# Optimization experiments

Measured on AMD Instinct MI355X. Metric: run time of the kernel, lower is better.

Reference implementation:

```python
import jax, jax.numpy as jnp
import numpy as np

H = 16      # num_attention_heads
D = 128     # head_size
ROT = 32    # rotary_ndims
WIN = 256   # attention_window[layer_id]
G = 64      # max_global_tokens
BASE = 10000.0


def _rotate_half(x):
    x1, x2 = jnp.split(x, 2, axis=-1)
    return jnp.concatenate([-x2, x1], axis=-1)


def setup_inputs() -> dict:
    key = jax.random.key(0)
    ks = jax.random.split(key, 6)
    B, S, HD = 2, 2048, H * D
    hidden_states = jax.random.normal(ks[0], (B, S, HD), jnp.float32)
    attention_mask = jnp.zeros((B, 1, 1, S), jnp.float32)
    glob_idx = jnp.sort(jax.random.randint(ks[1], (B, G), 0, S), axis=-1)
    W_qkv = jax.random.normal(ks[2], (HD, 3 * HD), jnp.float32) * 0.02
    b_qkv = jnp.zeros((3 * HD,), jnp.float32)
    W_o = jax.random.normal(ks[3], (HD, HD), jnp.float32) * 0.02
    b_o = jnp.zeros((HD,), jnp.float32)
    return {"hidden_states": hidden_states, "attention_mask": attention_mask,
            "glob_idx": glob_idx, "W_qkv": W_qkv, "b_qkv": b_qkv,
            "W_o": W_o, "b_o": b_o}


def reference(hidden_states, attention_mask, glob_idx, W_qkv, b_qkv, W_o, b_o):
    B, S, HD = hidden_states.shape
    qkv = (hidden_states @ W_qkv + b_qkv).reshape(B, S, H, 3 * D)
    q = qkv[..., :D].transpose(0, 2, 1, 3)        # [B,H,S,D]
    k = qkv[..., D:2 * D].transpose(0, 2, 1, 3)
    v = qkv[..., 2 * D:].transpose(0, 2, 1, 3)

    # GPT-NeoX rotary on first ROT dims
    inv_freq = 1.0 / (BASE ** (jnp.arange(0, ROT, 2, dtype=jnp.float32) / ROT))
    freqs = jnp.einsum('s,f->sf', jnp.arange(S, dtype=jnp.float32), inv_freq)
    emb = jnp.concatenate([freqs, freqs], axis=-1)           # [S,ROT]
    cos = jnp.cos(emb)[None, None]
    sin = jnp.sin(emb)[None, None]
    q = jnp.concatenate([q[..., :ROT] * cos + _rotate_half(q[..., :ROT]) * sin,
                         q[..., ROT:]], axis=-1)
    k = jnp.concatenate([k[..., :ROT] * cos + _rotate_half(k[..., :ROT]) * sin,
                         k[..., ROT:]], axis=-1)

    # step_attn path: keys/values are head-averaged before attention (key.mean(1))
    k_mean = k.mean(axis=1)   # [B,S,D]
    v_mean = v.mean(axis=1)
    scale = 1.0 / jnp.sqrt(jnp.float32(D))
    minv = jnp.finfo(jnp.float32).min

    s0 = jnp.einsum('bhqd,bkd->bhqk', q[:, :, :WIN], k_mean[:, :WIN]) * scale
    causal = jnp.tril(jnp.ones((WIN, WIN), bool))
    s0 = jnp.where(causal[None, None], s0, minv) + attention_mask[..., :WIN]
    out0 = jnp.einsum('bhqk,bkd->bhqd', jax.nn.softmax(s0, axis=-1), v_mean[:, :WIN])

    Sq = S - WIN
    steps = jnp.arange(Sq)
    win_pos = steps[:, None] + 1 + jnp.arange(WIN)[None, :]
    k_win = k_mean[:, win_pos]
    v_win = v_mean[:, win_pos]
    mask_win = attention_mask[:, 0, 0, :][:, win_pos][:, None]
    qs = q[:, :, WIN:]                                        # [B,H,Sq,D]
    s_win = jnp.einsum('bhqd,bqwd->bhqw', qs, k_win) * scale + mask_win

    k_glob = jnp.take_along_axis(k_mean, glob_idx[..., None], axis=1)  # [B,G,D]
    v_glob = jnp.take_along_axis(v_mean, glob_idx[..., None], axis=1)
    # sorted indices: 'filter < i then truncate to G' == prefix-valid mask per slot
    valid = (glob_idx[:, None, :] < steps[None, :, None])[:, None]     # [B,1,Sq,G]
    s_glob = jnp.where(valid, jnp.einsum('bhqd,bgd->bhqg', qs, k_glob) * scale, minv)

    w = jax.nn.softmax(jnp.concatenate([s_glob, s_win], axis=-1), axis=-1)
    out_steps = (jnp.einsum('bhqg,bgd->bhqd', w[..., :G], v_glob)
                 + jnp.einsum('bhqw,bqwd->bhqd', w[..., G:], v_win))

    out = jnp.concatenate([out0, out_steps], axis=2)          # [B,H,S,D]
    out = out.transpose(0, 2, 1, 3).reshape(B, S, HD)
    return out @ W_o + b_o
```

## Files before the change

kernel.cpp:

```cpp
#include <hip/hip_runtime.h>
#include <math.h>

#define SCALE_ 0.08838834764831845f
#define MINV_  (-3.4028234663852886e38f)

typedef __bf16 bf16;
typedef bf16  bf16x4 __attribute__((ext_vector_type(4)));
typedef bf16  bf16x8 __attribute__((ext_vector_type(8)));
typedef float f32x4  __attribute__((ext_vector_type(4)));
typedef float f32x16 __attribute__((ext_vector_type(16)));
typedef float float4v __attribute__((ext_vector_type(4)));

#define LD8(p) (*(const bf16x8*)(p))

__device__ __forceinline__ f32x4 mfma16(bf16x8 a, bf16x8 b, f32x4 c) {
    return __builtin_amdgcn_mfma_f32_16x16x32_bf16(a, b, c, 0, 0, 0);
}
__device__ __forceinline__ f32x16 mfma32(bf16x8 a, bf16x8 b, f32x16 c) {
    return __builtin_amdgcn_mfma_f32_32x32x16_bf16(a, b, c, 0, 0, 0);
}

typedef const __attribute__((address_space(1))) void* gas_t;
typedef __attribute__((address_space(3))) void* sas_t;
__device__ __forceinline__ void gload_lds16(const void* g, void* l) {
    __builtin_amdgcn_global_load_lds((gas_t)g, (sas_t)l, 16, 0, 0);
}

__global__ __launch_bounds__(256) void prep_kernel(const float* __restrict__ hidden, bf16* __restrict__ A16,
                                                   const float* __restrict__ Wqkv, bf16* __restrict__ BT1,
                                                   const float* __restrict__ Wo, bf16* __restrict__ BT2,
                                                   const float* __restrict__ bqkv, float* __restrict__ bias1)
{
    int x = blockIdx.x;
    if (x < 512) {
        int k0 = x * 4;
        int j = threadIdx.x;
        float acc[4];
        #pragma unroll
        for (int k = 0; k < 4; k++) acc[k] = 0.f;
        for (int h = 0; h < 16; h++) {
            #pragma unroll
            for (int k = 0; k < 4; k++)
                acc[k] += Wqkv[(size_t)(k0 + k) * 6144 + h * 384 + 128 + j];
        }
        #pragma unroll
        for (int k = 0; k < 4; k++)
            BT1[(size_t)(2048 + j) * 2048 + k0 + k] = (bf16)(acc[k] * 0.0625f);
        return;
    }
    if (x == 512) {
        for (int c = threadIdx.x; c < 2304; c += 256) {
            if (c < 2048) bias1[c] = bqkv[(c >> 7) * 384 + (c & 127)];
            else {
                int j = c - 2048; float s = 0.f;
                for (int h = 0; h < 16; h++) s += bqkv[h * 384 + 128 + j];
                bias1[c] = s * 0.0625f;
            }
        }
        return;
    }
    if (x < 8705) {
        int i = ((x - 513) * 256 + threadIdx.x) * 4;
        float4v v = *(const float4v*)(hidden + i);
        bf16x4 o; o.x = (bf16)v.x; o.y = (bf16)v.y; o.z = (bf16)v.z; o.w = (bf16)v.w;
        *(bf16x4*)(A16 + i) = o;
        return;
    }
    __shared__ float tile[32][33];
    int t = x - 8705;
    int z = t >> 12;
    int tt = t & 4095;
    const float* W = z ? Wo : Wqkv;
    bf16* BT = z ? BT2 : BT1;
    int srcStride = z ? 2048 : 6144;
    int k0 = (tt & 63) * 32, n0 = (tt >> 6) * 32;
    int c = threadIdx.x & 31, r = threadIdx.x >> 5;
    int n = n0 + c;
    int src = z ? n : ((n >> 7) * 384 + (n & 127));
    #pragma unroll
    for (int rr = 0; rr < 32; rr += 8)
        tile[r + rr][c] = W[(size_t)(k0 + r + rr) * srcStride + src];
    __syncthreads();
    #pragma unroll
    for (int rr = 0; rr < 32; rr += 8)
        BT[(size_t)(n0 + r + rr) * 2048 + k0 + c] = (bf16)tile[c][r + rr];
}


#define GEMM64K128_PROLOGUE_AND_KLOOP                                                     \
    __shared__ __align__(16) bf16 As[128 * 128];                                          \
    __shared__ __align__(16) bf16 Bs[64 * 128];                                           \
    const int tid  = threadIdx.x;                                                         \
    const int wv   = tid >> 6, lane = tid & 63, l32 = lane & 31, half = lane >> 5;        \
    const int m0 = blockIdx.y * 128, n0 = blockIdx.x * 64;                                \
    int rowSA[8], colSA[8];                                                               \
    _Pragma("unroll")                                                                     \
    for (int j = 0; j < 8; j++) {                                                         \
        int flat = (wv * 8 + j) * 64 + lane;                                              \
        rowSA[j] = flat >> 4;                                                             \
        colSA[j] = ((flat & 15) ^ (rowSA[j] & 15)) * 8;                                   \
    }                                                                                     \
    int rowSB[4], colSB[4];                                                               \
    _Pragma("unroll")                                                                     \
    for (int j = 0; j < 4; j++) {                                                         \
        int flat = (wv * 4 + j) * 64 + lane;                                              \
        rowSB[j] = flat >> 4;                                                             \
        colSB[j] = ((flat & 15) ^ (rowSB[j] & 15)) * 8;                                   \
    }                                                                                     \
    f32x16 acc[2];                                                                        \
    _Pragma("unroll")                                                                     \
    for (int i = 0; i < 2; i++)                                                           \
        _Pragma("unroll")                                                                 \
        for (int r = 0; r < 16; r++) acc[i][r] = 0.f;                                     \
    for (int kk = 0; kk < K; kk += 128) {                                                 \
        __syncthreads();                                                                  \
        _Pragma("unroll")                                                                 \
        for (int j = 0; j < 8; j++)                                                       \
            gload_lds16(A  + (size_t)(m0 + rowSA[j]) * K + kk + colSA[j], &As[(wv * 8 + j) * 512]); \
        _Pragma("unroll")                                                                 \
        for (int j = 0; j < 4; j++)                                                       \
            gload_lds16(BT + (size_t)(n0 + rowSB[j]) * K + kk + colSB[j], &Bs[(wv * 4 + j) * 512]); \
        __syncthreads();                                                                  \
        const int rowA = wv * 32 + l32;                                                   \
        const int rowB0 = l32, rowB1 = 32 + l32;                                          \
        _Pragma("unroll")                                                                 \
        for (int k16 = 0; k16 < 8; k16++) {                                               \
            int lc = k16 * 2 + half;                                                      \
            bf16x8 af = LD8(&As[rowA * 128 + ((lc ^ (rowA & 15)) * 8)]);                  \
            bf16x8 b0 = LD8(&Bs[rowB0 * 128 + ((lc ^ (rowB0 & 15)) * 8)]);                \
            bf16x8 b1 = LD8(&Bs[rowB1 * 128 + ((lc ^ (rowB1 & 15)) * 8)]);                \
            acc[0] = mfma32(af, b0, acc[0]);                                              \
            acc[1] = mfma32(af, b1, acc[1]);                                              \
        }                                                                                 \
    }

__global__ __launch_bounds__(256) void gemm_rot_kernel(const bf16* __restrict__ A, const bf16* __restrict__ BT,
                                                       const float* __restrict__ bias, bf16* __restrict__ C,
                                                       int M, int N, int K)
{
    GEMM64K128_PROLOGUE_AND_KLOOP

    #pragma unroll
    for (int nt = 0; nt < 2; nt++) {
        int n = n0 + nt * 32 + l32;
        float bn = bias[n];
        const bool rot = ((n0 & 127) == 0) && (nt == 0) && (n0 <= 2048);
        float inv = rot ? __expf(-0.575646273248511f * (float)(l32 & 15)) : 0.f;
        #pragma unroll
        for (int r = 0; r < 16; r++) {
            int m = m0 + wv * 32 + (r & 3) + 8 * (r >> 2) + 4 * half;
            float v = acc[nt][r] + bn;
            if (rot) {
                float ang = (float)(m & 2047) * inv;
                float cs, sn;
                __sincosf(ang, &sn, &cs);
                float pv = __shfl_xor(v, 16, 64);
                v = (l32 < 16) ? (v * cs - pv * sn) : (v * cs + pv * sn);
            }
            C[(size_t)m * N + n] = (bf16)v;
        }
    }
}


__global__ __launch_bounds__(256) void gemm_out_kernel(const bf16* __restrict__ A, const bf16* __restrict__ BT,
                                                       const float* __restrict__ bias, float* __restrict__ C,
                                                       int M, int N, int K)
{
    __shared__ __align__(16) bf16 As[128 * 64];
    __shared__ __align__(16) bf16 Bs[128 * 64];
    const int tid  = threadIdx.x;
    const int wv   = tid >> 6, lane = tid & 63, l32 = lane & 31, half = lane >> 5;
    const int wrow = wv >> 1, wcol = wv & 1;
    const int m0 = blockIdx.y * 128, n0 = blockIdx.x * 128;
    int rowS[4], colS[4];
    #pragma unroll
    for (int j = 0; j < 4; j++) {
        int flat = (wv * 4 + j) * 64 + lane;
        int row = flat >> 3, cp = flat & 7;
        rowS[j] = row;
        colS[j] = (cp ^ (row & 7)) * 8;
    }
    f32x16 acc[2][2];
    #pragma unroll
    for (int i = 0; i < 2; i++)
        #pragma unroll
        for (int j = 0; j < 2; j++)
            #pragma unroll
            for (int r = 0; r < 16; r++) acc[i][j][r] = 0.f;
    for (int kk = 0; kk < K; kk += 64) {
        __syncthreads();
        #pragma unroll
        for (int j = 0; j < 4; j++) {
            gload_lds16(A  + (size_t)(m0 + rowS[j]) * K + kk + colS[j], &As[(wv * 4 + j) * 512]);
            gload_lds16(BT + (size_t)(n0 + rowS[j]) * K + kk + colS[j], &Bs[(wv * 4 + j) * 512]);
        }
        __syncthreads();
        bf16x8 af[2][4], bfr[2][4];
        #pragma unroll
        for (int mt = 0; mt < 2; mt++) {
            int row = wrow * 64 + mt * 32 + l32;
            #pragma unroll
            for (int k16 = 0; k16 < 4; k16++) {
                int lc = k16 * 2 + half;
                af[mt][k16] = LD8(&As[row * 64 + ((lc ^ (row & 7)) * 8)]);
            }
        }
        #pragma unroll
        for (int nt = 0; nt < 2; nt++) {
            int row = wcol * 64 + nt * 32 + l32;
            #pragma unroll
            for (int k16 = 0; k16 < 4; k16++) {
                int lc = k16 * 2 + half;
                bfr[nt][k16] = LD8(&Bs[row * 64 + ((lc ^ (row & 7)) * 8)]);
            }
        }
        #pragma unroll
        for (int k16 = 0; k16 < 4; k16++)
            #pragma unroll
            for (int mt = 0; mt < 2; mt++)
                #pragma unroll
                for (int nt = 0; nt < 2; nt++)
                    acc[mt][nt] = mfma32(af[mt][k16], bfr[nt][k16], acc[mt][nt]);
    }

    #pragma unroll
    for (int mt = 0; mt < 2; mt++) {
        #pragma unroll
        for (int nt = 0; nt < 2; nt++) {
            int n = n0 + wcol * 64 + nt * 32 + l32;
            float bn = bias[n];
            #pragma unroll
            for (int r = 0; r < 16; r++) {
                int m = m0 + wrow * 64 + mt * 32 + (r & 3) + 8 * (r >> 2) + 4 * half;
                C[(size_t)m * N + n] = acc[mt][nt][r] + bn;
            }
        }
    }
}

__global__ __launch_bounds__(256) void pretile_kernel(const bf16* __restrict__ C1, const int* __restrict__ gidx,
                                                      bf16* __restrict__ KF, bf16* __restrict__ VF)
{
    __shared__ bf16 Vt[64][130];
    const int c = blockIdx.x, b = blockIdx.y;
    const bool isGlob = (c == 32);
    const int tid = threadIdx.x;

    {
        int row = tid >> 2, cb = (tid & 3) * 32;
        int pos = isGlob ? gidx[b * 64 + row] : (c * 64 + row);
        const bf16* src = C1 + (size_t)(b * 2048 + pos) * 2304 + 2176 + cb;
        #pragma unroll
        for (int k = 0; k < 4; k++)
            *(bf16x8*)&Vt[row][cb + k * 8] = LD8(src + k * 8);
    }
    __syncthreads();

    #pragma unroll
    for (int i = 0; i < 4; i++) {
        int sid = tid + i * 256;
        int lane = sid & 63, fi = sid >> 6;
        int l16 = lane & 15, quad = lane >> 4;
        int t = fi >> 2, ks = fi & 3;
        int pos = isGlob ? gidx[b * 64 + t * 16 + l16] : (c * 64 + t * 16 + l16);
        const bf16* src = C1 + (size_t)(b * 2048 + pos) * 2304 + 2048 + ks * 32 + quad * 8;
        *(bf16x8*)&KF[((size_t)(b * 33 + c) * 16 + fi) * 512 + lane * 8] = LD8(src);
    }

    #pragma unroll
    for (int i = 0; i < 4; i++) {
        int sid = tid + i * 256;
        int lane = sid & 63, fi = sid >> 6;
        int l16 = lane & 15, quad = lane >> 4;
        int dt = fi >> 1, ks2 = fi & 1;
        int d = dt * 16 + l16;
        bf16x8 v;
        #pragma unroll
        for (int j = 0; j < 8; j++)
            v[j] = Vt[ks2 * 32 + quad * 8 + j][d];
        *(bf16x8*)&VF[((size_t)(b * 33 + c) * 16 + fi) * 512 + lane * 8] = v;
    }
}

#define PSTRIDE 88

__device__ __forceinline__ void attn0_body(int bx, int h, int b, bf16* Pw,
                                           const bf16* __restrict__ C1, const bf16* __restrict__ KF,
                                           const bf16* __restrict__ VF, const float* __restrict__ mask,
                                           bf16* __restrict__ attn)
{
    const int tid = threadIdx.x, wv = tid >> 6, lane = tid & 63, quad = lane >> 4, l16 = lane & 15;
    const int q0 = (bx * 4 + wv) * 16;

    bf16x8 af[4];
    const bf16* qbase = C1 + (size_t)(b * 2048 + q0 + l16) * 2304 + h * 128;
    #pragma unroll
    for (int ks = 0; ks < 4; ks++) af[ks] = LD8(qbase + ks * 32 + quad * 8);

    f32x4 m_run = (f32x4){MINV_, MINV_, MINV_, MINV_};
    f32x4 l_run = (f32x4){0.f, 0.f, 0.f, 0.f};
    f32x4 O[8];
    #pragma unroll
    for (int dt = 0; dt < 8; dt++) O[dt] = (f32x4){0.f, 0.f, 0.f, 0.f};

    for (int c = 0; c <= bx; c++) {
        const bf16* KFc = KF + ((size_t)(b * 33 + c) * 16) * 512;
        const bf16* VFc = VF + ((size_t)(b * 33 + c) * 16) * 512;

        f32x4 acc[4];
        #pragma unroll
        for (int t = 0; t < 4; t++) acc[t] = (f32x4){0.f, 0.f, 0.f, 0.f};
        #pragma unroll
        for (int t = 0; t < 4; t++)
            #pragma unroll
            for (int ks = 0; ks < 4; ks++)
                acc[t] = mfma16(af[ks], LD8(KFc + (size_t)(t * 4 + ks) * 512 + lane * 8), acc[t]);

        float sv[4][4];
        #pragma unroll
        for (int t = 0; t < 4; t++) {
            int key = c * 64 + t * 16 + l16;
            float addv = mask[b * 2048 + key];
            #pragma unroll
            for (int r = 0; r < 4; r++) {
                int q = q0 + quad * 4 + r;
                sv[t][r] = (key <= q) ? (acc[t][r] * SCALE_ + addv) : MINV_;
            }
        }

        f32x4 cm;
        #pragma unroll
        for (int r = 0; r < 4; r++) cm[r] = fmaxf(fmaxf(sv[0][r], sv[1][r]), fmaxf(sv[2][r], sv[3][r]));
        #pragma unroll
        for (int ms = 1; ms < 16; ms <<= 1)
            #pragma unroll
            for (int r = 0; r < 4; r++) cm[r] = fmaxf(cm[r], __shfl_xor(cm[r], ms, 64));

        f32x4 nm, alpha;
        #pragma unroll
        for (int r = 0; r < 4; r++) { nm[r] = fmaxf(m_run[r], cm[r]); alpha[r] = __expf(m_run[r] - nm[r]); }

        float pv[4][4];
        f32x4 cs = (f32x4){0.f, 0.f, 0.f, 0.f};
        #pragma unroll
        for (int t = 0; t < 4; t++)
            #pragma unroll
            for (int r = 0; r < 4; r++) {
                pv[t][r] = __expf(sv[t][r] - nm[r]);
                cs[r] += pv[t][r];
            }
        #pragma unroll
        for (int ms = 1; ms < 16; ms <<= 1)
            #pragma unroll
            for (int r = 0; r < 4; r++) cs[r] += __shfl_xor(cs[r], ms, 64);

        m_run = nm;
        #pragma unroll
        for (int r = 0; r < 4; r++) l_run[r] = l_run[r] * alpha[r] + cs[r];
        #pragma unroll
        for (int dt = 0; dt < 8; dt++)
            #pragma unroll
            for (int r = 0; r < 4; r++) O[dt][r] *= alpha[r];

        #pragma unroll
        for (int t = 0; t < 4; t++)
            #pragma unroll
            for (int r = 0; r < 4; r++)
                Pw[(quad * 4 + r) * PSTRIDE + t * 16 + l16] = (bf16)pv[t][r];
        bf16x8 pa0 = LD8(&Pw[l16 * PSTRIDE + quad * 8]);
        bf16x8 pa1 = LD8(&Pw[l16 * PSTRIDE + 32 + quad * 8]);

        #pragma unroll
        for (int dt = 0; dt < 8; dt++) {
            O[dt] = mfma16(pa0, LD8(VFc + (size_t)(dt * 2 + 0) * 512 + lane * 8), O[dt]);
            O[dt] = mfma16(pa1, LD8(VFc + (size_t)(dt * 2 + 1) * 512 + lane * 8), O[dt]);
        }
    }

    f32x4 invl;
    #pragma unroll
    for (int r = 0; r < 4; r++) invl[r] = 1.0f / l_run[r];
    #pragma unroll
    for (int dt = 0; dt < 8; dt++)
        #pragma unroll
        for (int r = 0; r < 4; r++) {
            int q = q0 + quad * 4 + r;
            attn[(size_t)(b * 2048 + q) * 2048 + h * 128 + dt * 16 + l16] = (bf16)(O[dt][r] * invl[r]);
        }
}

__device__ __forceinline__ void attn_steps_body(int sb, int b, bf16* Pw,
                                                const bf16* __restrict__ C1, const bf16* __restrict__ KF,
                                                const bf16* __restrict__ VF, const float* __restrict__ mask,
                                                const int* __restrict__ gidx, bf16* __restrict__ attn)
{
    const int tid = threadIdx.x, wv = tid >> 6, lane = tid & 63, quad = lane >> 4, l16 = lane & 15;
    const int step = sb * 4 + wv, p = 256 + step;

    bf16x8 af[4];
    const bf16* qrow = C1 + (size_t)(b * 2048 + p) * 2304;
    #pragma unroll
    for (int ks = 0; ks < 4; ks++) af[ks] = LD8(qrow + l16 * 128 + ks * 32 + quad * 8);

    int gix[4];
    #pragma unroll
    for (int t = 0; t < 4; t++) gix[t] = gidx[b * 64 + t * 16 + l16];

    f32x4 m_run = (f32x4){MINV_, MINV_, MINV_, MINV_};
    f32x4 l_run = (f32x4){0.f, 0.f, 0.f, 0.f};
    f32x4 O[8];
    #pragma unroll
    for (int dt = 0; dt < 8; dt++) O[dt] = (f32x4){0.f, 0.f, 0.f, 0.f};

    const int c0 = (step + 1) >> 6;

    for (int iter = 0; iter < 6; iter++) {
        int c;
        bool isGlob = (iter == 0);
        if (isGlob) c = 32;
        else { c = c0 + iter - 1; if (c > 31) break; }

        const bf16* KFc = KF + ((size_t)(b * 33 + c) * 16) * 512;
        const bf16* VFc = VF + ((size_t)(b * 33 + c) * 16) * 512;

        f32x4 acc[4];
        #pragma unroll
        for (int t = 0; t < 4; t++) acc[t] = (f32x4){0.f, 0.f, 0.f, 0.f};
        #pragma unroll
        for (int t = 0; t < 4; t++)
            #pragma unroll
            for (int ks = 0; ks < 4; ks++)
                acc[t] = mfma16(af[ks], LD8(KFc + (size_t)(t * 4 + ks) * 512 + lane * 8), acc[t]);

        float sv[4][4];
        bool vld[4];
        #pragma unroll
        for (int t = 0; t < 4; t++) {
            float addv = 0.f;
            if (isGlob) vld[t] = gix[t] < step;
            else {
                int pos = c * 64 + t * 16 + l16;
                vld[t] = (unsigned)(pos - step - 1) < 256u;
                addv = mask[b * 2048 + pos];
            }
            #pragma unroll
            for (int r = 0; r < 4; r++) sv[t][r] = vld[t] ? (acc[t][r] * SCALE_ + addv) : MINV_;
        }

        f32x4 cm;
        #pragma unroll
        for (int r = 0; r < 4; r++) cm[r] = fmaxf(fmaxf(sv[0][r], sv[1][r]), fmaxf(sv[2][r], sv[3][r]));
        #pragma unroll
        for (int ms = 1; ms < 16; ms <<= 1)
            #pragma unroll
            for (int r = 0; r < 4; r++) cm[r] = fmaxf(cm[r], __shfl_xor(cm[r], ms, 64));

        f32x4 nm, alpha;
        #pragma unroll
        for (int r = 0; r < 4; r++) { nm[r] = fmaxf(m_run[r], cm[r]); alpha[r] = __expf(m_run[r] - nm[r]); }

        float pv[4][4];
        f32x4 cs = (f32x4){0.f, 0.f, 0.f, 0.f};
        #pragma unroll
        for (int t = 0; t < 4; t++)
            #pragma unroll
            for (int r = 0; r < 4; r++) {
                pv[t][r] = vld[t] ? __expf(sv[t][r] - nm[r]) : 0.f;
                cs[r] += pv[t][r];
            }
        #pragma unroll
        for (int ms = 1; ms < 16; ms <<= 1)
            #pragma unroll
            for (int r = 0; r < 4; r++) cs[r] += __shfl_xor(cs[r], ms, 64);

        m_run = nm;
        #pragma unroll
        for (int r = 0; r < 4; r++) l_run[r] = l_run[r] * alpha[r] + cs[r];
        #pragma unroll
        for (int dt = 0; dt < 8; dt++)
            #pragma unroll
            for (int r = 0; r < 4; r++) O[dt][r] *= alpha[r];

        #pragma unroll
        for (int t = 0; t < 4; t++)
            #pragma unroll
            for (int r = 0; r < 4; r++)
                Pw[(quad * 4 + r) * PSTRIDE + t * 16 + l16] = (bf16)pv[t][r];
        bf16x8 pa0 = LD8(&Pw[l16 * PSTRIDE + quad * 8]);
        bf16x8 pa1 = LD8(&Pw[l16 * PSTRIDE + 32 + quad * 8]);

        #pragma unroll
        for (int dt = 0; dt < 8; dt++) {
            O[dt] = mfma16(pa0, LD8(VFc + (size_t)(dt * 2 + 0) * 512 + lane * 8), O[dt]);
            O[dt] = mfma16(pa1, LD8(VFc + (size_t)(dt * 2 + 1) * 512 + lane * 8), O[dt]);
        }
    }

    f32x4 invl;
    #pragma unroll
    for (int r = 0; r < 4; r++) invl[r] = 1.0f / l_run[r];
    #pragma unroll
    for (int dt = 0; dt < 8; dt++)
        #pragma unroll
        for (int r = 0; r < 4; r++) {
            int h = quad * 4 + r;
            attn[(size_t)(b * 2048 + p) * 2048 + h * 128 + dt * 16 + l16] = (bf16)(O[dt][r] * invl[r]);
        }
}

__global__ __launch_bounds__(256) void attn_all_kernel(const bf16* __restrict__ C1, const bf16* __restrict__ KF,
                                                       const bf16* __restrict__ VF, const float* __restrict__ mask,
                                                       const int* __restrict__ gidx, bf16* __restrict__ attn)
{
    __shared__ __align__(16) bf16 Ps[4 * 16 * PSTRIDE];
    const int wv = threadIdx.x >> 6;
    bf16* Pw = &Ps[wv * (16 * PSTRIDE)];
    if (blockIdx.x < 448) {
        attn_steps_body(blockIdx.x, blockIdx.y, Pw, C1, KF, VF, mask, gidx, attn);
    } else {
        int bi = blockIdx.x - 448;
        attn0_body(bi >> 4, bi & 15, blockIdx.y, Pw, C1, KF, VF, mask, attn);
    }
}

extern "C" void kernel_launch(void* const* d_in, const int* in_sizes, int n_in,
                              void* d_out, int out_size, void* d_ws, size_t ws_size,
                              hipStream_t stream)
{
    const float* hidden = (const float*)d_in[0];
    const float* amask  = (const float*)d_in[1];
    const int*   gidx   = (const int*)d_in[2];
    const float* Wqkv   = (const float*)d_in[3];
    const float* bqkv   = (const float*)d_in[4];
    const float* Wo     = (const float*)d_in[5];
    const float* bo     = (const float*)d_in[6];

    char* ws = (char*)d_ws;
    size_t off = 0;
    auto take = [&](size_t bytes) -> char* {
        char* p = ws + off;
        off = (off + bytes + 255) & ~(size_t)255;
        return p;
    };
    bf16*  A16   = (bf16*)take(4096ull * 2048 * 2);
    bf16*  BT1   = (bf16*)take(2304ull * 2048 * 2);
    bf16*  BT2   = (bf16*)take(2048ull * 2048 * 2);
    bf16*  C1    = (bf16*)take(4096ull * 2304 * 2);
    bf16*  KF    = (bf16*)take(2ull * 33 * 16 * 512 * 2);
    bf16*  VF    = (bf16*)take(2ull * 33 * 16 * 512 * 2);
    bf16*  attnb = (bf16*)take(4096ull * 2048 * 2);
    float* bias1 = (float*)take(2304 * 4);

    prep_kernel<<<16897, 256, 0, stream>>>(hidden, A16, Wqkv, BT1, Wo, BT2, bqkv, bias1);

    gemm_rot_kernel<<<dim3(36, 32), 256, 0, stream>>>(A16, BT1, bias1, C1, 4096, 2304, 2048);

    pretile_kernel<<<dim3(33, 2), 256, 0, stream>>>(C1, gidx, KF, VF);

    attn_all_kernel<<<dim3(512, 2), 256, 0, stream>>>(C1, KF, VF, amask, gidx, attnb);

    gemm_out_kernel<<<dim3(16, 32), 256, 0, stream>>>(attnb, BT2, bo, (float*)d_out, 4096, 2048, 2048);

    (void)in_sizes; (void)n_in; (void)out_size; (void)ws_size;
}
```

Baseline: 293.7 us.

## Double-buffer LDS tiles in QKV GEMM with 64-wide K prefetch

Replaces the single-buffered 128-wide K loop of the QKV/rotary GEMM with a two-stage LDS ping-pong using 64-wide K tiles. The next tile's global-to-LDS loads are issued before the current tile's MFMAs, so load latency can overlap compute. Fragments are loaded into registers before the MFMA chain, and one barrier per iteration replaces two. In exchange it runs twice as many loop iterations with smaller tiles, slightly changes LDS usage, and raises register pressure.

```diff
diff --git a/kernel.cpp b/kernel.cpp
--- a/kernel.cpp
+++ b/kernel.cpp
@@ -87,58 +87,80 @@
 }
 
 
-#define GEMM64K128_PROLOGUE_AND_KLOOP                                                     \
-    __shared__ __align__(16) bf16 As[128 * 128];                                          \
-    __shared__ __align__(16) bf16 Bs[64 * 128];                                           \
-    const int tid  = threadIdx.x;                                                         \
-    const int wv   = tid >> 6, lane = tid & 63, l32 = lane & 31, half = lane >> 5;        \
-    const int m0 = blockIdx.y * 128, n0 = blockIdx.x * 64;                                \
-    int rowSA[8], colSA[8];                                                               \
-    _Pragma("unroll")                                                                     \
-    for (int j = 0; j < 8; j++) {                                                         \
-        int flat = (wv * 8 + j) * 64 + lane;                                              \
-        rowSA[j] = flat >> 4;                                                             \
-        colSA[j] = ((flat & 15) ^ (rowSA[j] & 15)) * 8;                                   \
-    }                                                                                     \
-    int rowSB[4], colSB[4];                                                               \
-    _Pragma("unroll")                                                                     \
-    for (int j = 0; j < 4; j++) {                                                         \
-        int flat = (wv * 4 + j) * 64 + lane;                                              \
-        rowSB[j] = flat >> 4;                                                             \
-        colSB[j] = ((flat & 15) ^ (rowSB[j] & 15)) * 8;                                   \
-    }                                                                                     \
-    f32x16 acc[2];                                                                        \
-    _Pragma("unroll")                                                                     \
-    for (int i = 0; i < 2; i++)                                                           \
-        _Pragma("unroll")                                                                 \
-        for (int r = 0; r < 16; r++) acc[i][r] = 0.f;                                     \
-    for (int kk = 0; kk < K; kk += 128) {                                                 \
-        __syncthreads();                                                                  \
-        _Pragma("unroll")                                                                 \
-        for (int j = 0; j < 8; j++)                                                       \
-            gload_lds16(A  + (size_t)(m0 + rowSA[j]) * K + kk + colSA[j], &As[(wv * 8 + j) * 512]); \
-        _Pragma("unroll")                                                                 \
-        for (int j = 0; j < 4; j++)                                                       \
-            gload_lds16(BT + (size_t)(n0 + rowSB[j]) * K + kk + colSB[j], &Bs[(wv * 4 + j) * 512]); \
-        __syncthreads();                                                                  \
-        const int rowA = wv * 32 + l32;                                                   \
-        const int rowB0 = l32, rowB1 = 32 + l32;                                          \
-        _Pragma("unroll")                                                                 \
-        for (int k16 = 0; k16 < 8; k16++) {                                               \
-            int lc = k16 * 2 + half;                                                      \
-            bf16x8 af = LD8(&As[rowA * 128 + ((lc ^ (rowA & 15)) * 8)]);                  \
-            bf16x8 b0 = LD8(&Bs[rowB0 * 128 + ((lc ^ (rowB0 & 15)) * 8)]);                \
-            bf16x8 b1 = LD8(&Bs[rowB1 * 128 + ((lc ^ (rowB1 & 15)) * 8)]);                \
-            acc[0] = mfma32(af, b0, acc[0]);                                              \
-            acc[1] = mfma32(af, b1, acc[1]);                                              \
-        }                                                                                 \
-    }
-
 __global__ __launch_bounds__(256) void gemm_rot_kernel(const bf16* __restrict__ A, const bf16* __restrict__ BT,
                                                        const float* __restrict__ bias, bf16* __restrict__ C,
                                                        int M, int N, int K)
 {
-    GEMM64K128_PROLOGUE_AND_KLOOP
+    __shared__ __align__(16) bf16 As[2][128 * 64];
+    __shared__ __align__(16) bf16 Bs[2][64 * 64];
+    const int tid  = threadIdx.x;
+    const int wv   = tid >> 6, lane = tid & 63, l32 = lane & 31, half = lane >> 5;
+    const int m0 = blockIdx.y * 128, n0 = blockIdx.x * 64;
+
+    int rowSA[4], colSA[4];
+    #pragma unroll
+    for (int j = 0; j < 4; j++) {
+        int flat = (wv * 4 + j) * 64 + lane;
+        rowSA[j] = flat >> 3;
+        colSA[j] = ((flat & 7) ^ (rowSA[j] & 7)) * 8;
+    }
+    int rowSB[2], colSB[2];
+    #pragma unroll
+    for (int j = 0; j < 2; j++) {
+        int flat = (wv * 2 + j) * 64 + lane;
+        rowSB[j] = flat >> 3;
+        colSB[j] = ((flat & 7) ^ (rowSB[j] & 7)) * 8;
+    }
+
+    auto stage = [&](int kk, int bsel) {
+        #pragma unroll
+        for (int j = 0; j < 4; j++)
+            gload_lds16(A  + (size_t)(m0 + rowSA[j]) * K + kk + colSA[j], &As[bsel][(wv * 4 + j) * 512]);
+        #pragma unroll
+        for (int j = 0; j < 2; j++)
+            gload_lds16(BT + (size_t)(n0 + rowSB[j]) * K + kk + colSB[j], &Bs[bsel][(wv * 2 + j) * 512]);
+    };
+
+    f32x16 acc[2];
+    #pragma unroll
+    for (int i = 0; i < 2; i++)
+        #pragma unroll
+        for (int r = 0; r < 16; r++) acc[i][r] = 0.f;
+
+    stage(0, 0);
+    __syncthreads();
+
+    int cur = 0;
+    for (int kk = 0; kk < K; kk += 64) {
+        if (kk + 64 < K) stage(kk + 64, cur ^ 1);
+
+        const bf16* Ab = &As[cur][0];
+        const bf16* Bb = &Bs[cur][0];
+        const int rowA = wv * 32 + l32;
+        bf16x8 af[4], bfr[2][4];
+        #pragma unroll
+        for (int k16 = 0; k16 < 4; k16++) {
+            int lc = k16 * 2 + half;
+            af[k16] = LD8(&Ab[rowA * 64 + ((lc ^ (rowA & 7)) * 8)]);
+        }
+        #pragma unroll
+        for (int nt = 0; nt < 2; nt++) {
+            int rowB = nt * 32 + l32;
+            #pragma unroll
+            for (int k16 = 0; k16 < 4; k16++) {
+                int lc = k16 * 2 + half;
+                bfr[nt][k16] = LD8(&Bb[rowB * 64 + ((lc ^ (rowB & 7)) * 8)]);
+            }
+        }
+        #pragma unroll
+        for (int k16 = 0; k16 < 4; k16++)
+            #pragma unroll
+            for (int nt = 0; nt < 2; nt++)
+                acc[nt] = mfma32(af[k16], bfr[nt][k16], acc[nt]);
+
+        __syncthreads();
+        cur ^= 1;
+    }
 
     #pragma unroll
     for (int nt = 0; nt < 2; nt++) {
@@ -161,7 +183,6 @@
         }
     }
 }
-
 
 __global__ __launch_bounds__(256) void gemm_out_kernel(const bf16* __restrict__ A, const bf16* __restrict__ BT,
                                                        const float* __restrict__ bias, float* __restrict__ C,
```

After: 299.6 us. +2.0%, slower.
